# Performance work log

Measured on AMD Instinct MI355X. Metric: run time of the kernel, lower is better.

## Reference

```python
import jax, jax.numpy as jnp
import numpy as np

B, S, D, H = 4, 2048, 1024, 16
DK = D // H

def setup_inputs() -> dict:
    key = jax.random.key(0)
    ks = jax.random.split(key, 11)
    sc = 1.0 / np.sqrt(D)
    return {
        "query": jax.random.normal(ks[0], (B, S, D), jnp.float32),
        "key_": jax.random.normal(ks[1], (B, S, D), jnp.float32),
        "value": jax.random.normal(ks[2], (B, S, D), jnp.float32),
        "Wq": jax.random.normal(ks[3], (D, D), jnp.float32) * sc,
        "bq": jnp.zeros((D,), jnp.float32),
        "Wk": jax.random.normal(ks[4], (D, D), jnp.float32) * sc,
        "bk": jnp.zeros((D,), jnp.float32),
        "Wv": jax.random.normal(ks[5], (D, D), jnp.float32) * sc,
        "bv": jnp.zeros((D,), jnp.float32),
        "Wo": jax.random.normal(ks[6], (D, D), jnp.float32) * sc,
        "bo": jnp.zeros((D,), jnp.float32),
    }

def reference(query, key_, value, Wq, bq, Wk, bk, Wv, bv, Wo, bo):
    def proj(x, W, b):
        # [B,S,D] -> [B,H,S,DK]
        y = x @ W.T + b
        return y.reshape(B, S, H, DK).transpose(0, 2, 1, 3)
    q = proj(query, Wq, bq)
    k = proj(key_, Wk, bk)
    v = proj(value, Wv, bv)
    scores = jnp.einsum("bhqd,bhkd->bhqk", q, k) / jnp.sqrt(jnp.float32(DK))
    p = jax.nn.softmax(scores, axis=-1)
    x = jnp.einsum("bhqk,bhkd->bhqd", p, v)
    x = x.transpose(0, 2, 1, 3).reshape(B, S, D)
    return x @ Wo.T + bo
```

## Files before the change

### kernel.cpp

```cpp
#include <hip/hip_runtime.h>
#include <math.h>

#define Bc 4
#define Sc 2048
#define Dc 1024
#define Hc 16
#define DKc 64

#define QSCALE_L2E 0.1803368801f
#define ZINIT_L2E  -11.5415603f

typedef __bf16 bf16;
typedef __bf16 bf16x2 __attribute__((ext_vector_type(2)));
typedef __bf16 bf16x4 __attribute__((ext_vector_type(4)));
typedef __bf16 bf16x8 __attribute__((ext_vector_type(8)));
typedef float  floatx4 __attribute__((ext_vector_type(4)));
typedef float  floatx16 __attribute__((ext_vector_type(16)));

__device__ __forceinline__ void load_lds16(const void* g, void* l) {
    __builtin_amdgcn_global_load_lds((const __attribute__((address_space(1))) void*)g,
                                     (__attribute__((address_space(3))) void*)l, 16, 0, 0);
}

#define MFMA16(a, b, c) __builtin_amdgcn_mfma_f32_16x16x32_bf16(a, b, c, 0, 0, 0)
#define MFMA32(a, b, c) __builtin_amdgcn_mfma_f32_32x32x16_bf16(a, b, c, 0, 0, 0)

__device__ __forceinline__ float exp2_fast(float x) {
    float r;
    asm("v_exp_f32 %0, %1" : "=v"(r) : "v"(x));
    return r;
}


#define GSTAGE(slot, kk) do {                                                 \
    load_lds16(A + (size_t)(m0 + w * 16 + srow) * K + (kk) + scol,            \
               As + (slot) * 4096 + w * 512);                                 \
    load_lds16(W + (size_t)(n0 + w * 16 + srow) * K + (kk) + scol,            \
               Bs + (slot) * 4096 + w * 512);                                 \
    load_lds16(A + (size_t)(m0 + (w + 4) * 16 + srow) * K + (kk) + scol,      \
               As + (slot) * 4096 + (w + 4) * 512);                           \
    load_lds16(W + (size_t)(n0 + (w + 4) * 16 + srow) * K + (kk) + scol,      \
               Bs + (slot) * 4096 + (w + 4) * 512);                           \
} while (0)

#define GCOMP(slot) do {                                                      \
    const bf16* Ab = As + (slot) * 4096;                                      \
    const bf16* Bb = Bs + (slot) * 4096;                                      \
    const bf16x8 af0 = *(const bf16x8*)(Ab + (wm + fl) * 32 + fq * 8);        \
    const bf16x8 af1 = *(const bf16x8*)(Ab + (wm + 16 + fl) * 32 + fq * 8);   \
    const bf16x8 af2 = *(const bf16x8*)(Ab + (wm + 32 + fl) * 32 + fq * 8);   \
    const bf16x8 af3 = *(const bf16x8*)(Ab + (wm + 48 + fl) * 32 + fq * 8);   \
    const bf16x8 bg0 = *(const bf16x8*)(Bb + (wn + fl) * 32 + fq * 8);        \
    const bf16x8 bg1 = *(const bf16x8*)(Bb + (wn + 16 + fl) * 32 + fq * 8);   \
    const bf16x8 bg2 = *(const bf16x8*)(Bb + (wn + 32 + fl) * 32 + fq * 8);   \
    const bf16x8 bg3 = *(const bf16x8*)(Bb + (wn + 48 + fl) * 32 + fq * 8);   \
    acc[0][0] = MFMA16(af0, bg0, acc[0][0]); acc[0][1] = MFMA16(af0, bg1, acc[0][1]); \
    acc[0][2] = MFMA16(af0, bg2, acc[0][2]); acc[0][3] = MFMA16(af0, bg3, acc[0][3]); \
    acc[1][0] = MFMA16(af1, bg0, acc[1][0]); acc[1][1] = MFMA16(af1, bg1, acc[1][1]); \
    acc[1][2] = MFMA16(af1, bg2, acc[1][2]); acc[1][3] = MFMA16(af1, bg3, acc[1][3]); \
    acc[2][0] = MFMA16(af2, bg0, acc[2][0]); acc[2][1] = MFMA16(af2, bg1, acc[2][1]); \
    acc[2][2] = MFMA16(af2, bg2, acc[2][2]); acc[2][3] = MFMA16(af2, bg3, acc[2][3]); \
    acc[3][0] = MFMA16(af3, bg0, acc[3][0]); acc[3][1] = MFMA16(af3, bg1, acc[3][1]); \
    acc[3][2] = MFMA16(af3, bg2, acc[3][2]); acc[3][3] = MFMA16(af3, bg3, acc[3][3]); \
} while (0)

template<int MODE>
__device__ __forceinline__ void gemm_body(const bf16* __restrict__ A,
                                          const bf16* __restrict__ W,
                                          const float* __restrict__ bias,
                                          void* __restrict__ out,
                                          bf16* As, bf16* Bs,
                                          int m0, int n0) {
    constexpr int N = Dc, K = Dc;
    const int t  = threadIdx.x;
    const int w  = t >> 6;
    const int l  = t & 63;
    const int wm = (w >> 1) * 64;
    const int wn = (w & 1) * 64;
    const int srow = l >> 2;
    const int scol = (l & 3) * 8;
    const int fl = l & 15;
    const int fq = l >> 4;

    floatx4 acc[4][4];
#pragma unroll
    for (int i = 0; i < 4; i++)
#pragma unroll
        for (int j = 0; j < 4; j++)
            acc[i][j] = (floatx4){0.f, 0.f, 0.f, 0.f};

    GSTAGE(0, 0);
    GSTAGE(1, 32);

#pragma unroll 1
    for (int s = 0; s < 31; ++s) {
        asm volatile("s_waitcnt vmcnt(4)" ::: "memory");
        __builtin_amdgcn_s_barrier();
        __builtin_amdgcn_sched_barrier(0);
        if (s + 2 < 32) GSTAGE((s + 2) % 3, 32 * (s + 2));
        GCOMP(s % 3);
    }
    __syncthreads();
    GCOMP(1);

#pragma unroll
    for (int tn = 0; tn < 4; tn++) {
        const int n = n0 + wn + tn * 16 + fl;
        const float bv = bias[n];
#pragma unroll
        for (int tm = 0; tm < 4; tm++) {
            const int mb = m0 + wm + tm * 16 + fq * 4;
            if (MODE == 0) {
                float* O = (float*)out;
#pragma unroll
                for (int r = 0; r < 4; r++)
                    O[(size_t)(mb + r) * N + n] = acc[tm][tn][r] + bv;
            } else if (MODE == 1) {
                bf16* O = (bf16*)out;
#pragma unroll
                for (int r = 0; r < 4; r++)
                    O[(size_t)(mb + r) * N + n] = (bf16)(acc[tm][tn][r] + bv);
            } else {
                const int h = n >> 6, dk = n & 63;
                const int b = mb >> 11, s2 = mb & 2047;
                bf16* O = (bf16*)out + ((size_t)((b * Hc + h) * DKc + dk)) * Sc + s2;
                bf16x4 pk = {(bf16)(acc[tm][tn][0] + bv), (bf16)(acc[tm][tn][1] + bv),
                             (bf16)(acc[tm][tn][2] + bv), (bf16)(acc[tm][tn][3] + bv)};
                *(bf16x4*)O = pk;
            }
        }
    }
}

__global__ __launch_bounds__(256) void gemm_qkv(
    const bf16* __restrict__ Aq, const bf16* __restrict__ Ak, const bf16* __restrict__ Av,
    const bf16* __restrict__ Wqb, const bf16* __restrict__ Wkb, const bf16* __restrict__ Wvb,
    const float* __restrict__ bqs, const float* __restrict__ bk, const float* __restrict__ bv,
    bf16* __restrict__ Oq, bf16* __restrict__ Ok, bf16* __restrict__ Ov) {
    __shared__ bf16 As[3 * 128 * 32];
    __shared__ bf16 Bs[3 * 128 * 32];
    const int bid  = blockIdx.x;
    const int xcd  = bid & 7;
    const int slot = bid >> 3;
    const int x    = slot & 7;
    const int j    = slot >> 3;
    const int yg   = xcd + 8 * j;
    const int sel  = yg >> 6;
    const int y    = yg & 63;
    const int m0 = y * 128, n0 = x * 128;
    if (sel == 0)      gemm_body<1>(Aq, Wqb, bqs, Oq, As, Bs, m0, n0);
    else if (sel == 1) gemm_body<1>(Ak, Wkb, bk,  Ok, As, Bs, m0, n0);
    else               gemm_body<2>(Av, Wvb, bv,  Ov, As, Bs, m0, n0);
}

__global__ __launch_bounds__(256) void gemm_out_k(const bf16* __restrict__ A,
                                                  const bf16* __restrict__ W,
                                                  const float* __restrict__ bias,
                                                  float* __restrict__ out) {
    __shared__ bf16 As[3 * 128 * 32];
    __shared__ bf16 Bs[3 * 128 * 32];
    const int bid  = blockIdx.x;
    const int xcd  = bid & 7;
    const int slot = bid >> 3;
    const int x    = slot & 7;
    const int j    = slot >> 3;
    const int y    = xcd + 8 * j;
    gemm_body<0>(A, W, bias, out, As, Bs, y * 128, x * 128);
}


__device__ __forceinline__ unsigned pkpair(float a, float b) {
    union { bf16x2 v; unsigned u; } x;
    x.v = (bf16x2){(bf16)a, (bf16)b};
    return x.u;
}

__device__ __forceinline__ bf16x8 frag4(unsigned a, unsigned b, unsigned c, unsigned d) {
    union { unsigned u[4]; bf16x8 v; } x;
    x.u[0] = a; x.u[1] = b; x.u[2] = c; x.u[3] = d;
    return x.v;
}

__device__ __forceinline__ floatx16 splat16(float v) {
    floatx16 r;
#pragma unroll
    for (int i = 0; i < 16; ++i) r[i] = v;
    return r;
}

#define PSWAP(x, y) do {                                                      \
    auto _r = __builtin_amdgcn_permlane32_swap((int)(x), (int)(y), false, false); \
    (x) = (unsigned)_r[0]; (y) = (unsigned)_r[1];                             \
} while (0)

#define STAGE(dst, kt) do {                                                   \
    load_lds16(Kb + (size_t)((kt) + w * 16 + r8) * Dc + c8 * 8,               \
               &Kbuf[dst][w * 1024]);                                         \
    load_lds16(Kb + (size_t)((kt) + w * 16 + 8 + r8) * Dc + c8 * 8,           \
               &Kbuf[dst][w * 1024 + 512]);                                   \
    load_lds16(Vb + (size_t)(w * 16 + r8) * Sc + (kt) + c8 * 8,               \
               &Vbuf[dst][w * 1024]);                                         \
    load_lds16(Vb + (size_t)(w * 16 + 8 + r8) * Sc + (kt) + c8 * 8,           \
               &Vbuf[dst][w * 1024 + 512]);                                   \
} while (0)

#define QKT(d, T, SACC) do {                                                  \
    const bf16* Kp = &Kbuf[d][((T) * 32 + ky) * 64];                          \
    const bf16x8 kf0 = *(const bf16x8*)(Kp + ((b5 ^ sw7) * 8));               \
    const bf16x8 kf1 = *(const bf16x8*)(Kp + (((2 + b5) ^ sw7) * 8));         \
    const bf16x8 kf2 = *(const bf16x8*)(Kp + (((4 + b5) ^ sw7) * 8));         \
    const bf16x8 kf3 = *(const bf16x8*)(Kp + (((6 + b5) ^ sw7) * 8));         \
    __builtin_amdgcn_s_setprio(1);                                            \
    SACC = MFMA32(kf0, qf0, z16);                                             \
    SACC = MFMA32(kf1, qf1, SACC);                                            \
    SACC = MFMA32(kf2, qf2, SACC);                                            \
    SACC = MFMA32(kf3, qf3, SACC);                                            \
    __builtin_amdgcn_s_setprio(0);                                            \
} while (0)

#define SOFTX(SACC, PF0, PF1) do {                                            \
    const float p0  = exp2_fast(SACC[0]),  p1  = exp2_fast(SACC[1]);          \
    const float p2  = exp2_fast(SACC[2]),  p3  = exp2_fast(SACC[3]);          \
    const float p4  = exp2_fast(SACC[4]),  p5  = exp2_fast(SACC[5]);          \
    const float p6  = exp2_fast(SACC[6]),  p7  = exp2_fast(SACC[7]);          \
    const float p8  = exp2_fast(SACC[8]),  p9  = exp2_fast(SACC[9]);          \
    const float p10 = exp2_fast(SACC[10]), p11 = exp2_fast(SACC[11]);         \
    const float p12 = exp2_fast(SACC[12]), p13 = exp2_fast(SACC[13]);         \
    const float p14 = exp2_fast(SACC[14]), p15 = exp2_fast(SACC[15]);         \
    lsum += (((p0 + p1) + (p2 + p3)) + ((p4 + p5) + (p6 + p7)))               \
          + (((p8 + p9) + (p10 + p11)) + ((p12 + p13) + (p14 + p15)));        \
    unsigned d0 = pkpair(p0, p1),   d1 = pkpair(p2, p3);                      \
    unsigned d2 = pkpair(p4, p5),   d3 = pkpair(p6, p7);                      \
    PSWAP(d0, d2); PSWAP(d1, d3);                                             \
    PF0 = frag4(d0, d1, d2, d3);                                              \
    unsigned e0 = pkpair(p8, p9),   e1 = pkpair(p10, p11);                    \
    unsigned e2 = pkpair(p12, p13), e3 = pkpair(p14, p15);                    \
    PSWAP(e0, e2); PSWAP(e1, e3);                                             \
    PF1 = frag4(e0, e1, e2, e3);                                              \
} while (0)

#define PVT(d, T, PF0, PF1) do {                                              \
    const bf16* Va = &Vbuf[d][ky * 64];                                       \
    const bf16* Vc = Va + 32 * 64;                                            \
    const bf16x8 vf00 = *(const bf16x8*)(Va + (((((T) << 2) + b5) ^ sw7) * 8));      \
    const bf16x8 vf01 = *(const bf16x8*)(Va + (((((T) << 2) + 2 + b5) ^ sw7) * 8));  \
    const bf16x8 vf10 = *(const bf16x8*)(Vc + (((((T) << 2) + b5) ^ sw7) * 8));      \
    const bf16x8 vf11 = *(const bf16x8*)(Vc + (((((T) << 2) + 2 + b5) ^ sw7) * 8));  \
    __builtin_amdgcn_s_setprio(1);                                            \
    oa = MFMA32(vf00, PF0, oa);                                               \
    oa = MFMA32(vf01, PF1, oa);                                               \
    ob = MFMA32(vf10, PF0, ob);                                               \
    ob = MFMA32(vf11, PF1, ob);                                               \
    __builtin_amdgcn_s_setprio(0);                                            \
} while (0)

#define REGION(d) do {                                                        \
    QKT(d, 0, sacc0);                                                         \
    QKT(d, 1, sacc1);                                                         \
    SOFTX(sacc0, pa0, pa1);                                                   \
    PVT(d, 0, pa0, pa1);                                                      \
    SOFTX(sacc1, pb0, pb1);                                                   \
    PVT(d, 1, pb0, pb1);                                                      \
} while (0)

__global__ __launch_bounds__(256, 3) void attn_mfma(const bf16* __restrict__ Q,
                                                    const bf16* __restrict__ Kg,
                                                    const bf16* __restrict__ Vt,
                                                    bf16* __restrict__ X) {
    __shared__ bf16 Kbuf[2][64 * 64];
    __shared__ bf16 Vbuf[2][64 * 64];

    const int bh = blockIdx.x & 63;
    const int qb = blockIdx.x >> 6;
    const int b = bh >> 4, h = bh & 15;

    const int w   = threadIdx.x >> 6;
    const int l   = threadIdx.x & 63;
    const int ky  = l & 31;
    const int b5  = l >> 5;
    const int sw7 = l & 7;
    const int r8  = l >> 3;
    const int c8  = (l & 7) ^ r8;
    const int q0i = qb * 128 + w * 32;

    const bf16* Qb = Q  + (size_t)b * Sc * Dc + h * DKc;
    const bf16* Kb = Kg + (size_t)b * Sc * Dc + h * DKc;
    const bf16* Vb = Vt + (size_t)((b * Hc + h) * DKc) * Sc;

    const bf16* Qrow = Qb + (size_t)(q0i + ky) * Dc + 8 * b5;
    const bf16x8 qf0 = *(const bf16x8*)(Qrow);
    const bf16x8 qf1 = *(const bf16x8*)(Qrow + 16);
    const bf16x8 qf2 = *(const bf16x8*)(Qrow + 32);
    const bf16x8 qf3 = *(const bf16x8*)(Qrow + 48);

    const floatx16 z16 = splat16(ZINIT_L2E);
    floatx16 oa = splat16(0.f), ob = splat16(0.f);
    floatx16 sacc0, sacc1;
    bf16x8 pa0, pa1, pb0, pb1;
    float lsum = 0.f;

    STAGE(0, 0);
    __syncthreads();

#pragma unroll 1
    for (int kt = 0; kt < Sc; kt += 128) {
        STAGE(1, kt + 64);
        REGION(0);
        __syncthreads();
        if (kt + 128 < Sc) STAGE(0, kt + 128);
        REGION(1);
        __syncthreads();
    }

    lsum += __shfl_xor(lsum, 32);
    const float inv = 1.f / lsum;
    bf16* xp = X + ((size_t)(b * Sc + q0i + ky)) * Dc + h * DKc + b5 * 4;
#pragma unroll
    for (int g = 0; g < 4; ++g) {
        bf16x4 pa = {(bf16)(oa[4 * g + 0] * inv), (bf16)(oa[4 * g + 1] * inv),
                     (bf16)(oa[4 * g + 2] * inv), (bf16)(oa[4 * g + 3] * inv)};
        *(bf16x4*)(xp + g * 8) = pa;
        bf16x4 pb = {(bf16)(ob[4 * g + 0] * inv), (bf16)(ob[4 * g + 1] * inv),
                     (bf16)(ob[4 * g + 2] * inv), (bf16)(ob[4 * g + 3] * inv)};
        *(bf16x4*)(xp + 32 + g * 8) = pb;
    }
}

__global__ __launch_bounds__(256) void prep(
    const float* __restrict__ q, const float* __restrict__ k, const float* __restrict__ v,
    const float* __restrict__ wq, const float* __restrict__ wk,
    const float* __restrict__ wv, const float* __restrict__ wo,
    const float* __restrict__ bq,
    bf16* __restrict__ oq, bf16* __restrict__ ok, bf16* __restrict__ ov,
    bf16* __restrict__ w0, bf16* __restrict__ w1,
    bf16* __restrict__ w2, bf16* __restrict__ w3,
    float* __restrict__ bqs) {
    const int NQ = 3 * 8192;
    const int NW = 4 * 1024;
    int bid = blockIdx.x;
    if (bid < NQ) {
        const int sel = bid >> 13;
        const int i = (bid & 8191) * 256 + threadIdx.x;
        const float* src = sel == 0 ? q : sel == 1 ? k : v;
        bf16* dst = sel == 0 ? oq : sel == 1 ? ok : ov;
        const float4 vv = ((const float4*)src)[i];
        bf16x4 o = {(bf16)vv.x, (bf16)vv.y, (bf16)vv.z, (bf16)vv.w};
        ((bf16x4*)dst)[i] = o;
    } else if (bid < NQ + NW) {
        bid -= NQ;
        const int sel = bid >> 10;
        const int i = (bid & 1023) * 256 + threadIdx.x;
        const float* src = sel == 0 ? wq : sel == 1 ? wk : sel == 2 ? wv : wo;
        bf16* dst = sel == 0 ? w0 : sel == 1 ? w1 : sel == 2 ? w2 : w3;
        const float scale = sel == 0 ? QSCALE_L2E : 1.f;
        const float4 vv = ((const float4*)src)[i];
        bf16x4 o = {(bf16)(vv.x * scale), (bf16)(vv.y * scale),
                    (bf16)(vv.z * scale), (bf16)(vv.w * scale)};
        ((bf16x4*)dst)[i] = o;
    } else {
        const int i = (bid - NQ - NW) * 256 + threadIdx.x;
        if (i < Dc) bqs[i] = bq[i] * QSCALE_L2E;
    }
}

extern "C" void kernel_launch(void* const* d_in, const int* in_sizes, int n_in,
                              void* d_out, int out_size, void* d_ws, size_t ws_size,
                              hipStream_t stream) {
    const float* query = (const float*)d_in[0];
    const float* key_  = (const float*)d_in[1];
    const float* value = (const float*)d_in[2];
    const float* Wq    = (const float*)d_in[3];
    const float* bq    = (const float*)d_in[4];
    const float* Wk    = (const float*)d_in[5];
    const float* bk    = (const float*)d_in[6];
    const float* Wv    = (const float*)d_in[7];
    const float* bv    = (const float*)d_in[8];
    const float* Wo    = (const float*)d_in[9];
    const float* bo    = (const float*)d_in[10];

    const size_t nSD = (size_t)Bc * Sc * Dc;
    const size_t nWW = (size_t)Dc * Dc;

    char* ws = (char*)d_ws;
    bf16* qbf = (bf16*)ws;              ws += nSD * 2;
    bf16* kbf = (bf16*)ws;              ws += nSD * 2;
    bf16* vbf = (bf16*)ws;              ws += nSD * 2;
    bf16* wqb = (bf16*)ws;              ws += nWW * 2;
    bf16* wkb = (bf16*)ws;              ws += nWW * 2;
    bf16* wvb = (bf16*)ws;              ws += nWW * 2;
    bf16* wob = (bf16*)ws;              ws += nWW * 2;
    bf16* Qw  = (bf16*)ws;              ws += nSD * 2;
    bf16* Kw  = (bf16*)ws;              ws += nSD * 2;
    bf16* Vtw = (bf16*)ws;              ws += nSD * 2;
    bf16* Xw  = (bf16*)ws;              ws += nSD * 2;
    float* bqs = (float*)ws;            ws += Dc * 4;

    prep<<<3 * 8192 + 4 * 1024 + 4, 256, 0, stream>>>(
        query, key_, value, Wq, Wk, Wv, Wo, bq,
        qbf, kbf, vbf, wqb, wkb, wvb, wob, bqs);

    gemm_qkv<<<3 * (Bc * Sc / 128) * (Dc / 128), 256, 0, stream>>>(
        qbf, kbf, vbf, wqb, wkb, wvb, bqs, bk, bv, Qw, Kw, Vtw);

    attn_mfma<<<(Sc / 128) * Hc * Bc, 256, 0, stream>>>(Qw, Kw, Vtw, Xw);

    gemm_out_k<<<(Bc * Sc / 128) * (Dc / 128), 256, 0, stream>>>(
        Xw, wob, bo, (float*)d_out);
}
```

Before: 328.8 us.

## Fuse fp32-to-bf16 activation conversion into the QKV projection GEMM

The separate prep pass that converted query/key/value from fp32 to bf16 is removed. The QKV GEMM now loads fp32 activation tiles into registers, converts them to bf16 and writes them to LDS, while the weights still stream in through direct global-to-LDS loads in a three-slot pipeline. This avoids writing and re-reading three 16 MB bf16 intermediates. In exchange the GEMM reads twice as many activation bytes per tile, uses more registers, and its pipeline needs manual waitcnt and barrier handling.

```diff
diff --git a/kernel.cpp b/kernel.cpp
--- a/kernel.cpp
+++ b/kernel.cpp
@@ -22,6 +22,10 @@
                                      (__attribute__((address_space(3))) void*)l, 16, 0, 0);
 }
 
+__device__ __forceinline__ void store_lds16(void* l, bf16x8 v) {
+    *(__attribute__((address_space(3))) bf16x8*)l = v;
+}
+
 #define MFMA16(a, b, c) __builtin_amdgcn_mfma_f32_16x16x32_bf16(a, b, c, 0, 0, 0)
 #define MFMA32(a, b, c) __builtin_amdgcn_mfma_f32_32x32x16_bf16(a, b, c, 0, 0, 0)
 
@@ -31,17 +35,24 @@
     return r;
 }
 
-
-#define GSTAGE(slot, kk) do {                                                 \
-    load_lds16(A + (size_t)(m0 + w * 16 + srow) * K + (kk) + scol,            \
-               As + (slot) * 4096 + w * 512);                                 \
-    load_lds16(W + (size_t)(n0 + w * 16 + srow) * K + (kk) + scol,            \
-               Bs + (slot) * 4096 + w * 512);                                 \
-    load_lds16(A + (size_t)(m0 + (w + 4) * 16 + srow) * K + (kk) + scol,      \
-               As + (slot) * 4096 + (w + 4) * 512);                           \
-    load_lds16(W + (size_t)(n0 + (w + 4) * 16 + srow) * K + (kk) + scol,      \
-               Bs + (slot) * 4096 + (w + 4) * 512);                           \
-} while (0)
+__device__ __forceinline__ unsigned pkpair(float a, float b) {
+    union { bf16x2 v; unsigned u; } x;
+    x.v = (bf16x2){(bf16)a, (bf16)b};
+    return x.u;
+}
+
+__device__ __forceinline__ bf16x8 frag4(unsigned a, unsigned b, unsigned c, unsigned d) {
+    union { unsigned u[4]; bf16x8 v; } x;
+    x.u[0] = a; x.u[1] = b; x.u[2] = c; x.u[3] = d;
+    return x.v;
+}
+
+__device__ __forceinline__ floatx16 splat16(float v) {
+    floatx16 r;
+#pragma unroll
+    for (int i = 0; i < 16; ++i) r[i] = v;
+    return r;
+}
 
 #define GCOMP(slot) do {                                                      \
     const bf16* Ab = As + (slot) * 4096;                                      \
@@ -64,6 +75,131 @@
     acc[3][2] = MFMA16(af3, bg2, acc[3][2]); acc[3][3] = MFMA16(af3, bg3, acc[3][3]); \
 } while (0)
 
+#define GEMM_EPILOGUE(MODE) do {                                              \
+    _Pragma("unroll")                                                         \
+    for (int tn = 0; tn < 4; tn++) {                                          \
+        const int n = n0 + wn + tn * 16 + fl;                                 \
+        const float bv = bias[n];                                             \
+        _Pragma("unroll")                                                     \
+        for (int tm = 0; tm < 4; tm++) {                                      \
+            const int mb = m0 + wm + tm * 16 + fq * 4;                        \
+            if (MODE == 0) {                                                  \
+                float* O = (float*)out;                                       \
+                _Pragma("unroll")                                             \
+                for (int r = 0; r < 4; r++)                                   \
+                    O[(size_t)(mb + r) * Dc + n] = acc[tm][tn][r] + bv;       \
+            } else if (MODE == 1) {                                           \
+                bf16* O = (bf16*)out;                                         \
+                _Pragma("unroll")                                             \
+                for (int r = 0; r < 4; r++)                                   \
+                    O[(size_t)(mb + r) * Dc + n] = (bf16)(acc[tm][tn][r] + bv); \
+            } else {                                                          \
+                const int h = n >> 6, dk = n & 63;                            \
+                const int b = mb >> 11, s2 = mb & 2047;                       \
+                bf16* O = (bf16*)out + ((size_t)((b * Hc + h) * DKc + dk)) * Sc + s2; \
+                bf16x4 pk = {(bf16)(acc[tm][tn][0] + bv), (bf16)(acc[tm][tn][1] + bv), \
+                             (bf16)(acc[tm][tn][2] + bv), (bf16)(acc[tm][tn][3] + bv)}; \
+                *(bf16x4*)O = pk;                                             \
+            }                                                                 \
+        }                                                                     \
+    }                                                                         \
+} while (0)
+
+
+#define FA_ISSUE(kk) do {                                                     \
+    const float* _p0 = Afp + (size_t)(m0 + w * 16 + srow) * Dc + (kk) + scol; \
+    const float* _p1 = Afp + (size_t)(m0 + (w + 4) * 16 + srow) * Dc + (kk) + scol; \
+    a0lo = *(const float4*)_p0; a0hi = *(const float4*)(_p0 + 4);             \
+    a1lo = *(const float4*)_p1; a1hi = *(const float4*)(_p1 + 4);             \
+} while (0)
+
+#define FW_ISSUE(slot, kk) do {                                               \
+    load_lds16(W + (size_t)(n0 + w * 16 + srow) * Dc + (kk) + scol,           \
+               Bs + (slot) * 4096 + w * 512);                                 \
+    load_lds16(W + (size_t)(n0 + (w + 4) * 16 + srow) * Dc + (kk) + scol,     \
+               Bs + (slot) * 4096 + (w + 4) * 512);                           \
+} while (0)
+
+#define FA_WRITE(slot) do {                                                   \
+    bf16x8 _v0 = frag4(pkpair(a0lo.x, a0lo.y), pkpair(a0lo.z, a0lo.w),        \
+                       pkpair(a0hi.x, a0hi.y), pkpair(a0hi.z, a0hi.w));       \
+    bf16x8 _v1 = frag4(pkpair(a1lo.x, a1lo.y), pkpair(a1lo.z, a1lo.w),        \
+                       pkpair(a1hi.x, a1hi.y), pkpair(a1hi.z, a1hi.w));       \
+    store_lds16(As + (slot) * 4096 + w * 512 + l * 8, _v0);                   \
+    store_lds16(As + (slot) * 4096 + (w + 4) * 512 + l * 8, _v1);             \
+} while (0)
+
+template<int MODE>
+__device__ __forceinline__ void gemm_fused_body(const float* __restrict__ Afp,
+                                                const bf16* __restrict__ W,
+                                                const float* __restrict__ bias,
+                                                void* __restrict__ out,
+                                                bf16* As, bf16* Bs,
+                                                int m0, int n0) {
+    const int t  = threadIdx.x;
+    const int w  = t >> 6;
+    const int l  = t & 63;
+    const int wm = (w >> 1) * 64;
+    const int wn = (w & 1) * 64;
+    const int srow = l >> 2;
+    const int scol = (l & 3) * 8;
+    const int fl = l & 15;
+    const int fq = l >> 4;
+
+    floatx4 acc[4][4];
+#pragma unroll
+    for (int i = 0; i < 4; i++)
+#pragma unroll
+        for (int j = 0; j < 4; j++)
+            acc[i][j] = (floatx4){0.f, 0.f, 0.f, 0.f};
+
+    float4 a0lo, a0hi, a1lo, a1hi;
+
+    FA_ISSUE(0); FW_ISSUE(0, 0);
+    FA_WRITE(0);
+    __builtin_amdgcn_sched_barrier(0);
+    FA_ISSUE(32); FW_ISSUE(1, 32);
+    __builtin_amdgcn_sched_barrier(0);
+    asm volatile("s_waitcnt vmcnt(6)" ::: "memory");
+    asm volatile("s_waitcnt lgkmcnt(0)" ::: "memory");
+    __builtin_amdgcn_s_barrier();
+    __builtin_amdgcn_sched_barrier(0);
+
+#pragma unroll 1
+    for (int s = 0; s < 30; ++s) {
+        FA_WRITE((s + 1) % 3);
+        __builtin_amdgcn_sched_barrier(0);
+        FA_ISSUE(32 * (s + 2)); FW_ISSUE((s + 2) % 3, 32 * (s + 2));
+        __builtin_amdgcn_sched_barrier(0);
+        GCOMP(s % 3);
+        __builtin_amdgcn_sched_barrier(0);
+        asm volatile("s_waitcnt vmcnt(6)" ::: "memory");
+        asm volatile("s_waitcnt lgkmcnt(0)" ::: "memory");
+        __builtin_amdgcn_s_barrier();
+        __builtin_amdgcn_sched_barrier(0);
+    }
+    FA_WRITE(1);
+    __builtin_amdgcn_sched_barrier(0);
+    GCOMP(0);
+    __builtin_amdgcn_sched_barrier(0);
+    asm volatile("s_waitcnt vmcnt(0) lgkmcnt(0)" ::: "memory");
+    __builtin_amdgcn_s_barrier();
+    GCOMP(1);
+
+    GEMM_EPILOGUE(MODE);
+}
+
+#define GSTAGE(slot, kk) do {                                                 \
+    load_lds16(A + (size_t)(m0 + w * 16 + srow) * Dc + (kk) + scol,           \
+               As + (slot) * 4096 + w * 512);                                 \
+    load_lds16(W + (size_t)(n0 + w * 16 + srow) * Dc + (kk) + scol,           \
+               Bs + (slot) * 4096 + w * 512);                                 \
+    load_lds16(A + (size_t)(m0 + (w + 4) * 16 + srow) * Dc + (kk) + scol,     \
+               As + (slot) * 4096 + (w + 4) * 512);                           \
+    load_lds16(W + (size_t)(n0 + (w + 4) * 16 + srow) * Dc + (kk) + scol,     \
+               Bs + (slot) * 4096 + (w + 4) * 512);                           \
+} while (0)
+
 template<int MODE>
 __device__ __forceinline__ void gemm_body(const bf16* __restrict__ A,
                                           const bf16* __restrict__ W,
@@ -71,7 +207,6 @@
                                           void* __restrict__ out,
                                           bf16* As, bf16* Bs,
                                           int m0, int n0) {
-    constexpr int N = Dc, K = Dc;
     const int t  = threadIdx.x;
     const int w  = t >> 6;
     const int l  = t & 63;
@@ -103,37 +238,11 @@
     __syncthreads();
     GCOMP(1);
 
-#pragma unroll
-    for (int tn = 0; tn < 4; tn++) {
-        const int n = n0 + wn + tn * 16 + fl;
-        const float bv = bias[n];
-#pragma unroll
-        for (int tm = 0; tm < 4; tm++) {
-            const int mb = m0 + wm + tm * 16 + fq * 4;
-            if (MODE == 0) {
-                float* O = (float*)out;
-#pragma unroll
-                for (int r = 0; r < 4; r++)
-                    O[(size_t)(mb + r) * N + n] = acc[tm][tn][r] + bv;
-            } else if (MODE == 1) {
-                bf16* O = (bf16*)out;
-#pragma unroll
-                for (int r = 0; r < 4; r++)
-                    O[(size_t)(mb + r) * N + n] = (bf16)(acc[tm][tn][r] + bv);
-            } else {
-                const int h = n >> 6, dk = n & 63;
-                const int b = mb >> 11, s2 = mb & 2047;
-                bf16* O = (bf16*)out + ((size_t)((b * Hc + h) * DKc + dk)) * Sc + s2;
-                bf16x4 pk = {(bf16)(acc[tm][tn][0] + bv), (bf16)(acc[tm][tn][1] + bv),
-                             (bf16)(acc[tm][tn][2] + bv), (bf16)(acc[tm][tn][3] + bv)};
-                *(bf16x4*)O = pk;
-            }
-        }
-    }
+    GEMM_EPILOGUE(MODE);
 }
 
 __global__ __launch_bounds__(256) void gemm_qkv(
-    const bf16* __restrict__ Aq, const bf16* __restrict__ Ak, const bf16* __restrict__ Av,
+    const float* __restrict__ Aq, const float* __restrict__ Ak, const float* __restrict__ Av,
     const bf16* __restrict__ Wqb, const bf16* __restrict__ Wkb, const bf16* __restrict__ Wvb,
     const float* __restrict__ bqs, const float* __restrict__ bk, const float* __restrict__ bv,
     bf16* __restrict__ Oq, bf16* __restrict__ Ok, bf16* __restrict__ Ov) {
@@ -148,9 +257,9 @@
     const int sel  = yg >> 6;
     const int y    = yg & 63;
     const int m0 = y * 128, n0 = x * 128;
-    if (sel == 0)      gemm_body<1>(Aq, Wqb, bqs, Oq, As, Bs, m0, n0);
-    else if (sel == 1) gemm_body<1>(Ak, Wkb, bk,  Ok, As, Bs, m0, n0);
-    else               gemm_body<2>(Av, Wvb, bv,  Ov, As, Bs, m0, n0);
+    if (sel == 0)      gemm_fused_body<1>(Aq, Wqb, bqs, Oq, As, Bs, m0, n0);
+    else if (sel == 1) gemm_fused_body<1>(Ak, Wkb, bk,  Ok, As, Bs, m0, n0);
+    else               gemm_fused_body<2>(Av, Wvb, bv,  Ov, As, Bs, m0, n0);
 }
 
 __global__ __launch_bounds__(256) void gemm_out_k(const bf16* __restrict__ A,
@@ -168,25 +277,6 @@
     gemm_body<0>(A, W, bias, out, As, Bs, y * 128, x * 128);
 }
 
-
-__device__ __forceinline__ unsigned pkpair(float a, float b) {
-    union { bf16x2 v; unsigned u; } x;
-    x.v = (bf16x2){(bf16)a, (bf16)b};
-    return x.u;
-}
-
-__device__ __forceinline__ bf16x8 frag4(unsigned a, unsigned b, unsigned c, unsigned d) {
-    union { unsigned u[4]; bf16x8 v; } x;
-    x.u[0] = a; x.u[1] = b; x.u[2] = c; x.u[3] = d;
-    return x.v;
-}
-
-__device__ __forceinline__ floatx16 splat16(float v) {
-    floatx16 r;
-#pragma unroll
-    for (int i = 0; i < 16; ++i) r[i] = v;
-    return r;
-}
 
 #define PSWAP(x, y) do {                                                      \
     auto _r = __builtin_amdgcn_permlane32_swap((int)(x), (int)(y), false, false); \
@@ -327,27 +417,15 @@
 }
 
 __global__ __launch_bounds__(256) void prep(
-    const float* __restrict__ q, const float* __restrict__ k, const float* __restrict__ v,
     const float* __restrict__ wq, const float* __restrict__ wk,
     const float* __restrict__ wv, const float* __restrict__ wo,
     const float* __restrict__ bq,
-    bf16* __restrict__ oq, bf16* __restrict__ ok, bf16* __restrict__ ov,
     bf16* __restrict__ w0, bf16* __restrict__ w1,
     bf16* __restrict__ w2, bf16* __restrict__ w3,
     float* __restrict__ bqs) {
-    const int NQ = 3 * 8192;
     const int NW = 4 * 1024;
     int bid = blockIdx.x;
-    if (bid < NQ) {
-        const int sel = bid >> 13;
-        const int i = (bid & 8191) * 256 + threadIdx.x;
-        const float* src = sel == 0 ? q : sel == 1 ? k : v;
-        bf16* dst = sel == 0 ? oq : sel == 1 ? ok : ov;
-        const float4 vv = ((const float4*)src)[i];
-        bf16x4 o = {(bf16)vv.x, (bf16)vv.y, (bf16)vv.z, (bf16)vv.w};
-        ((bf16x4*)dst)[i] = o;
-    } else if (bid < NQ + NW) {
-        bid -= NQ;
+    if (bid < NW) {
         const int sel = bid >> 10;
         const int i = (bid & 1023) * 256 + threadIdx.x;
         const float* src = sel == 0 ? wq : sel == 1 ? wk : sel == 2 ? wv : wo;
@@ -358,7 +436,7 @@
                     (bf16)(vv.z * scale), (bf16)(vv.w * scale)};
         ((bf16x4*)dst)[i] = o;
     } else {
-        const int i = (bid - NQ - NW) * 256 + threadIdx.x;
+        const int i = (bid - NW) * 256 + threadIdx.x;
         if (i < Dc) bqs[i] = bq[i] * QSCALE_L2E;
     }
 }
@@ -382,9 +460,6 @@
     const size_t nWW = (size_t)Dc * Dc;
 
     char* ws = (char*)d_ws;
-    bf16* qbf = (bf16*)ws;              ws += nSD * 2;
-    bf16* kbf = (bf16*)ws;              ws += nSD * 2;
-    bf16* vbf = (bf16*)ws;              ws += nSD * 2;
     bf16* wqb = (bf16*)ws;              ws += nWW * 2;
     bf16* wkb = (bf16*)ws;              ws += nWW * 2;
     bf16* wvb = (bf16*)ws;              ws += nWW * 2;
@@ -395,12 +470,11 @@
     bf16* Xw  = (bf16*)ws;              ws += nSD * 2;
     float* bqs = (float*)ws;            ws += Dc * 4;
 
-    prep<<<3 * 8192 + 4 * 1024 + 4, 256, 0, stream>>>(
-        query, key_, value, Wq, Wk, Wv, Wo, bq,
-        qbf, kbf, vbf, wqb, wkb, wvb, wob, bqs);
+    prep<<<4 * 1024 + 4, 256, 0, stream>>>(
+        Wq, Wk, Wv, Wo, bq, wqb, wkb, wvb, wob, bqs);
 
     gemm_qkv<<<3 * (Bc * Sc / 128) * (Dc / 128), 256, 0, stream>>>(
-        qbf, kbf, vbf, wqb, wkb, wvb, bqs, bk, bv, Qw, Kw, Vtw);
+        query, key_, value, wqb, wkb, wvb, bqs, bk, bv, Qw, Kw, Vtw);
 
     attn_mfma<<<(Sc / 128) * Hc * Bc, 256, 0, stream>>>(Qw, Kw, Vtw, Xw);
 
```

After: 379.8 us. +15.5%, slower.
